# Kernel tuning notes

Measured on AMD Instinct MI355X. Metric: run time of the kernel, lower is better.

## Reference

```python
import jax, jax.numpy as jnp
import numpy as np

B, S, E, H, FFN, NQ, DEPTH = 2, 2048, 1024, 16, 4096, 4, 2
DK = E // H
LN_EPS = 1e-5


def _layernorm(t, g, b):
    m = t.mean(-1, keepdims=True)
    v = ((t - m) ** 2).mean(-1, keepdims=True)
    return (t - m) / jnp.sqrt(v + LN_EPS) * g + b


def setup_inputs() -> dict:
    key = jax.random.key(0)
    ks = jax.random.split(key, 12)
    n = lambda i, shape, sc=1.0: (jax.random.normal(ks[i], shape, jnp.float32) * sc)
    return {
        "x": n(0, (B, S, E)),
        "wq": n(1, (E, E), 0.02),
        "wk": n(2, (E, E), 0.02),
        "wv": n(3, (E, E), 0.02),
        "wo": n(4, (E, E), 0.02),
        "w1": n(5, (E, FFN), 0.02),
        "b1": jnp.zeros((FFN,), jnp.float32),
        "w2": n(6, (FFN, E), 0.02),
        "b2": jnp.zeros((E,), jnp.float32),
        "qp_attn": n(7, (NQ, DEPTH)),
        "qp_ffn": n(8, (NQ, DEPTH)),
        "ln1_g": jnp.ones((E,), jnp.float32),
        "ln1_b": jnp.zeros((E,), jnp.float32),
        "ln2_g": jnp.ones((E,), jnp.float32),
        "ln2_b": jnp.zeros((E,), jnp.float32),
    }


def reference(x, wq, wk, wv, wo, w1, b1, w2, b2, qp_attn, qp_ffn,
              ln1_g, ln1_b, ln2_g, ln2_b):
    b, s, _ = x.shape
    # --- quantum attention ---
    q = (x @ wq).reshape(b, s, H, DK)
    k = (x @ wk).reshape(b, s, H, DK)
    v = (x @ wv).reshape(b, s, H, DK)
    scores = jnp.einsum('bqhd,bkhd->bhqk', q, k) / np.sqrt(DK).astype(np.float32)
    attn = jax.nn.softmax(scores, axis=-1)
    classical = jnp.einsum('bhqk,bkhd->bqhd', attn, v)  # (b, s, H, DK)
    # depth-2 RX-only circuit on |0..0>: <Z_0> = cos(sum_d params[0, d]);
    # data-independent scalar broadcast to the first NQ channels of each head
    c_attn = jnp.cos(qp_attn[0].sum())
    mixed = classical.at[..., :NQ].add(c_attn)
    attn_out = mixed.reshape(b, s, E) @ wo
    x1 = _layernorm(x + attn_out, ln1_g, ln1_b)  # dropout is identity in eval
    # --- quantum feed-forward ---
    h = x1 @ w1 + b1  # computed in the source but never consumed by the circuit
    # depth-2 RY-only circuit: <Z_0> = cos(sum_d params[0, d]) -- also data-free
    c_ffn = jnp.cos(qp_ffn[0].sum())
    qvec = jnp.zeros((FFN,), x.dtype).at[:NQ].set(c_ffn)
    ffn_out = jax.nn.relu(qvec) @ w2 + b2  # (E,), broadcast per token
    return _layernorm(x1 + ffn_out, ln2_g, ln2_b)
```

## Files before the change

### kernel.cpp

```cpp
#include <hip/hip_runtime.h>
#include <hip/hip_bf16.h>

typedef unsigned short u16;
using short8 = __attribute__((ext_vector_type(8))) short;
using f32x4  = __attribute__((ext_vector_type(4))) float;

#define S_  2048
#define E_  1024
#define H_  16
#define DK_ 64

#define GLP(p)  ((const __attribute__((address_space(1))) void*)(p))
#define LDSP(p) ((__attribute__((address_space(3))) void*)(p))

__device__ __forceinline__ float b2f(u16 u) {
  union { unsigned int i; float f; } v; v.i = ((unsigned int)u) << 16; return v.f;
}
__device__ __forceinline__ u16 f2b(float f) {
  union { float f; unsigned int i; } v; v.f = f;
  unsigned int r = v.i + 0x7fffu + ((v.i >> 16) & 1u);
  return (u16)(r >> 16);
}
__device__ __forceinline__ unsigned pk2(float a, float b) {
  __hip_bfloat162 h = __float22bfloat162_rn(make_float2(a, b));
  union { __hip_bfloat162 h; unsigned u; } c; c.h = h; return c.u;
}
__device__ __forceinline__ float fexp2(float x) {
#if __has_builtin(__builtin_amdgcn_exp2f)
  return __builtin_amdgcn_exp2f(x);
#else
  return exp2f(x);
#endif
}

__global__ __launch_bounds__(256) void prep_k(
    const float* __restrict__ x,
    const float* __restrict__ wq, const float* __restrict__ wk,
    const float* __restrict__ wv, const float* __restrict__ wo,
    const float* __restrict__ w2, const float* __restrict__ b2,
    const float* __restrict__ qpf,
    u16* __restrict__ xb, u16* __restrict__ wt, float* __restrict__ fv) {
  __shared__ u16 tile[64][65];
  int id = blockIdx.x, t = threadIdx.x;
  if (id < 2048) {
    size_t i = ((size_t)id * 256 + t) * 8;
    float4 a = *(const float4*)&x[i];
    float4 b = *(const float4*)&x[i + 4];
    uint4 o;
    o.x = pk2(a.x, a.y); o.y = pk2(a.z, a.w);
    o.z = pk2(b.x, b.y); o.w = pk2(b.z, b.w);
    *(uint4*)&xb[i] = o;
  } else if (id < 3072) {
    int i = id - 2048;
    int z = i >> 8; i &= 255;
    const float* src = (z == 0) ? wq : (z == 1) ? wk : (z == 2) ? wv : wo;
    u16* dst = wt + (size_t)z * E_ * E_;
    int k0 = (i & 15) * 64, n0 = (i >> 4) * 64;
    int rr = t >> 4, c4 = (t & 15) * 4;
    for (int p = 0; p < 4; p++) {
      int r = p * 16 + rr;
      float4 v = *(const float4*)&src[(size_t)(k0 + r) * E_ + n0 + c4];
      tile[r][c4] = f2b(v.x); tile[r][c4 + 1] = f2b(v.y);
      tile[r][c4 + 2] = f2b(v.z); tile[r][c4 + 3] = f2b(v.w);
    }
    __syncthreads();
    for (int p = 0; p < 4; p++) {
      int r = p * 16 + rr;
      ushort4 o;
      o.x = tile[c4][r]; o.y = tile[c4 + 1][r]; o.z = tile[c4 + 2][r]; o.w = tile[c4 + 3][r];
      *(ushort4*)&dst[(size_t)(n0 + r) * E_ + k0 + c4] = o;
    }
  } else {
    int e = (id - 3072) * 256 + t;
    float r = fmaxf(cosf(qpf[0] + qpf[1]), 0.f);
    fv[e] = b2[e] + r * (w2[0 * E_ + e] + w2[1 * E_ + e] + w2[2 * E_ + e] + w2[3 * E_ + e]);
  }
}

__device__ __forceinline__ void gemm_loop97(
    const u16* __restrict__ A, const u16* __restrict__ Bt,
    int m0, int n0, f32x4 acc[4][4], u16 (*As)[128][32], u16 (*Bs)[128][32]) {
  int t = threadIdx.x, lane = t & 63, w = t >> 6;
  int wm = w >> 1, wn = w & 1, l15 = lane & 15, quad = lane >> 4;
  int srow = lane >> 2, sch = (lane & 3) * 8;
  const u16 *ga[2], *gb[2];
#pragma unroll
  for (int p = 0; p < 2; p++) {
    int seg = w * 2 + p;
    ga[p] = A + (size_t)(m0 + seg * 16 + srow) * E_ + sch;
    gb[p] = Bt + (size_t)(n0 + seg * 16 + srow) * E_ + sch;
  }
#pragma unroll
  for (int p = 0; p < 2; p++) {
    int seg = w * 2 + p;
    __builtin_amdgcn_global_load_lds(GLP(ga[p]), LDSP(&As[0][seg * 16][0]), 16, 0, 0);
    __builtin_amdgcn_global_load_lds(GLP(gb[p]), LDSP(&Bs[0][seg * 16][0]), 16, 0, 0);
    ga[p] += 32; gb[p] += 32;
  }
  for (int i = 0; i < 32; i++) {
    __syncthreads();
    if (i + 1 < 32) {
      int nb = (i + 1) & 1;
#pragma unroll
      for (int p = 0; p < 2; p++) {
        int seg = w * 2 + p;
        __builtin_amdgcn_global_load_lds(GLP(ga[p]), LDSP(&As[nb][seg * 16][0]), 16, 0, 0);
        __builtin_amdgcn_global_load_lds(GLP(gb[p]), LDSP(&Bs[nb][seg * 16][0]), 16, 0, 0);
        ga[p] += 32; gb[p] += 32;
      }
    }
    int cb = i & 1;
    short8 af[4], bf[4];
#pragma unroll
    for (int ii = 0; ii < 4; ii++) af[ii] = *(const short8*)&As[cb][wm * 64 + ii * 16 + l15][quad * 8];
#pragma unroll
    for (int j = 0; j < 4; j++) bf[j] = *(const short8*)&Bs[cb][wn * 64 + j * 16 + l15][quad * 8];
#pragma unroll
    for (int ii = 0; ii < 4; ii++)
#pragma unroll
      for (int j = 0; j < 4; j++)
        acc[ii][j] = __builtin_amdgcn_mfma_f32_16x16x32_bf16(af[ii], bf[j], acc[ii][j], 0, 0, 0);
  }
}

__global__ __launch_bounds__(256) void qkv_gemm(
    const u16* __restrict__ xb, const u16* __restrict__ wt,
    u16* __restrict__ q, u16* __restrict__ k, u16* __restrict__ vt) {
  __shared__ __align__(16) u16 As[2][128][32];
  __shared__ __align__(16) u16 Bs[2][128][32];
  int n0 = blockIdx.x * 128, m0 = blockIdx.y * 128, z = blockIdx.z;
  const u16* Bt = wt + (size_t)z * E_ * E_;
  f32x4 acc[4][4];
  f32x4 zero = {0.f, 0.f, 0.f, 0.f};
  for (int i = 0; i < 4; i++)
    for (int j = 0; j < 4; j++) acc[i][j] = zero;
  gemm_loop97(xb, Bt, m0, n0, acc, As, Bs);
  int t = threadIdx.x, lane = t & 63, w = t >> 6;
  int wm = w >> 1, wn = w & 1, l15 = lane & 15, quad = lane >> 4;
  if (z < 2) {
    u16* out = (z == 0) ? q : k;
    float sc = (z == 0) ? 0.18033688f : 1.f;
#pragma unroll
    for (int i = 0; i < 4; i++)
#pragma unroll
      for (int j = 0; j < 4; j++) {
        int mm = m0 + wm * 64 + i * 16 + quad * 4;
        int nn = n0 + wn * 64 + j * 16 + l15;
#pragma unroll
        for (int rr = 0; rr < 4; rr++)
          out[(size_t)(mm + rr) * E_ + nn] = f2b(acc[i][j][rr] * sc);
      }
  } else {
#pragma unroll
    for (int i = 0; i < 4; i++)
#pragma unroll
      for (int j = 0; j < 4; j++) {
        int mm = m0 + wm * 64 + i * 16 + quad * 4;
        int nn = n0 + wn * 64 + j * 16 + l15;
        int b = mm >> 11, s = mm & (S_ - 1);
        size_t base = ((size_t)(b * H_ + (nn >> 6)) * DK_ + (nn & 63)) * S_ + s;
        ushort4 pk;
        pk.x = f2b(acc[i][j][0]); pk.y = f2b(acc[i][j][1]);
        pk.z = f2b(acc[i][j][2]); pk.w = f2b(acc[i][j][3]);
        *(ushort4*)&vt[base] = pk;
      }
  }
}

__global__ __launch_bounds__(256) void oproj_gemm(
    const u16* __restrict__ am, const u16* __restrict__ wot, float* __restrict__ proj) {
  __shared__ __align__(16) u16 As[2][128][32];
  __shared__ __align__(16) u16 Bs[2][128][32];
  int n0 = blockIdx.x * 128, m0 = blockIdx.y * 128;
  f32x4 acc[4][4];
  f32x4 zero = {0.f, 0.f, 0.f, 0.f};
  for (int i = 0; i < 4; i++)
    for (int j = 0; j < 4; j++) acc[i][j] = zero;
  gemm_loop97(am, wot, m0, n0, acc, As, Bs);
  int t = threadIdx.x, lane = t & 63, w = t >> 6;
  int wm = w >> 1, wn = w & 1, l15 = lane & 15, quad = lane >> 4;
#pragma unroll
  for (int i = 0; i < 4; i++)
#pragma unroll
    for (int j = 0; j < 4; j++) {
      int mm = m0 + wm * 64 + i * 16 + quad * 4;
      int nn = n0 + wn * 64 + j * 16 + l15;
#pragma unroll
      for (int rr = 0; rr < 4; rr++)
        proj[(size_t)(mm + rr) * E_ + nn] = acc[i][j][rr];
    }
}

__global__ __launch_bounds__(256, 3) void attn_kernel(
    const u16* __restrict__ q, const u16* __restrict__ kk,
    const u16* __restrict__ vt, const float* __restrict__ qpa,
    u16* __restrict__ outm) {
  __shared__ __align__(16) u16 QPs[128][64];
  __shared__ __align__(16) u16 Ks[2][64][64];
  __shared__ __align__(16) u16 Vts[2][64][64];
  int qt = blockIdx.x, bh = blockIdx.y;
  int b = bh >> 4, h = bh & 15;
  int q0 = qt * 128;
  int t = threadIdx.x, lane = t & 63, w = t >> 6;
  int l15 = lane & 15, quad = lane >> 4;
  float c_attn = cosf(qpa[0] + qpa[1]);
  int r8 = lane >> 3, slot = lane & 7;
  size_t kbase = (size_t)(b * S_) * E_ + h * DK_;
  size_t vbase = (size_t)(b * H_ + h) * DK_ * S_;
#pragma unroll
  for (int p = 0; p < 4; p++) {
    int row = w * 32 + p * 8 + r8;
    int c = slot ^ (row & 7);
    const u16* gq = q + (size_t)(b * S_ + q0 + row) * E_ + h * DK_ + c * 8;
    __builtin_amdgcn_global_load_lds(GLP(gq), LDSP(&QPs[w * 32 + p * 8][0]), 16, 0, 0);
  }
  const u16 *kptr[2], *vptr[2];
#pragma unroll
  for (int p = 0; p < 2; p++) {
    int row = w * 16 + p * 8 + r8;
    int c = slot ^ (row & 7);
    kptr[p] = kk + kbase + (size_t)row * E_ + c * 8;
    vptr[p] = vt + vbase + (size_t)row * S_ + c * 8;
    __builtin_amdgcn_global_load_lds(GLP(kptr[p]), LDSP(&Ks[0][w * 16 + p * 8][0]), 16, 0, 0);
    __builtin_amdgcn_global_load_lds(GLP(vptr[p]), LDSP(&Vts[0][w * 16 + p * 8][0]), 16, 0, 0);
    kptr[p] += (size_t)64 * E_;
    vptr[p] += 64;
  }
  __syncthreads();
  short8 bq[2][2];
#pragma unroll
  for (int nb = 0; nb < 2; nb++) {
    int row = w * 32 + nb * 16 + l15;
    int c0 = quad ^ (row & 7);
    bq[nb][0] = *(const short8*)&QPs[row][c0 * 8];
    bq[nb][1] = *(const short8*)&QPs[row][(c0 ^ 4) * 8];
  }
  short8 bones;
#pragma unroll
  for (int i = 0; i < 8; i++) bones[i] = (short)0x3F80;
  f32x4 O[2][4], Osum[2];
  f32x4 zero = {0.f, 0.f, 0.f, 0.f};
#pragma unroll
  for (int i = 0; i < 2; i++) {
    Osum[i] = zero;
#pragma unroll
    for (int j = 0; j < 4; j++) O[i][j] = zero;
  }
  for (int kt = 0; kt < S_ / 64; kt++) {
    if (kt) __syncthreads();
    if (kt + 1 < S_ / 64) {
      int nb2 = (kt + 1) & 1;
#pragma unroll
      for (int p = 0; p < 2; p++) {
        __builtin_amdgcn_global_load_lds(GLP(kptr[p]), LDSP(&Ks[nb2][w * 16 + p * 8][0]), 16, 0, 0);
        __builtin_amdgcn_global_load_lds(GLP(vptr[p]), LDSP(&Vts[nb2][w * 16 + p * 8][0]), 16, 0, 0);
        kptr[p] += (size_t)64 * E_;
        vptr[p] += 64;
      }
    }
    int cb = kt & 1;
    f32x4 sc[4][2];
#pragma unroll
    for (int mb = 0; mb < 4; mb++) {
      int row = mb * 16 + l15;
      int c0 = quad ^ (row & 7);
      short8 a0 = *(const short8*)&Ks[cb][row][c0 * 8];
      short8 a1 = *(const short8*)&Ks[cb][row][(c0 ^ 4) * 8];
#pragma unroll
      for (int nb = 0; nb < 2; nb++) {
        f32x4 z = __builtin_amdgcn_mfma_f32_16x16x32_bf16(a0, bq[nb][0], zero, 0, 0, 0);
        sc[mb][nb] = __builtin_amdgcn_mfma_f32_16x16x32_bf16(a1, bq[nb][1], z, 0, 0, 0);
      }
    }
#pragma unroll
    for (int mb = 0; mb < 4; mb++)
#pragma unroll
      for (int nb = 0; nb < 2; nb++) {
        float p0 = fexp2(sc[mb][nb][0]);
        float p1 = fexp2(sc[mb][nb][1]);
        float p2 = fexp2(sc[mb][nb][2]);
        float p3 = fexp2(sc[mb][nb][3]);
        unsigned pa = pk2(p0, p1), pb = pk2(p2, p3);
        int row = nb * 16 + l15;
        int cch = (mb * 2 + (quad >> 1)) ^ (row & 7);
        uint2 pw; pw.x = pa; pw.y = pb;
        *(uint2*)&QPs[w * 32 + row][cch * 8 + (quad & 1) * 4] = pw;
      }
    asm volatile("s_waitcnt lgkmcnt(0)" ::: "memory");
    short8 bv[4][2];
#pragma unroll
    for (int nd = 0; nd < 4; nd++) {
      int rv = nd * 16 + l15;
      int cv = quad ^ (rv & 7);
      bv[nd][0] = *(const short8*)&Vts[cb][rv][cv * 8];
      bv[nd][1] = *(const short8*)&Vts[cb][rv][(cv ^ 4) * 8];
    }
#pragma unroll
    for (int mbq = 0; mbq < 2; mbq++) {
      int row = mbq * 16 + l15;
      int s0 = quad ^ (row & 7);
      int s1 = (4 + quad) ^ (row & 7);
      short8 ap0 = *(const short8*)&QPs[w * 32 + row][s0 * 8];
      short8 ap1 = *(const short8*)&QPs[w * 32 + row][s1 * 8];
#pragma unroll
      for (int nd = 0; nd < 4; nd++) {
        O[mbq][nd] = __builtin_amdgcn_mfma_f32_16x16x32_bf16(ap0, bv[nd][0], O[mbq][nd], 0, 0, 0);
        O[mbq][nd] = __builtin_amdgcn_mfma_f32_16x16x32_bf16(ap1, bv[nd][1], O[mbq][nd], 0, 0, 0);
      }
      Osum[mbq] = __builtin_amdgcn_mfma_f32_16x16x32_bf16(ap0, bones, Osum[mbq], 0, 0, 0);
      Osum[mbq] = __builtin_amdgcn_mfma_f32_16x16x32_bf16(ap1, bones, Osum[mbq], 0, 0, 0);
    }
  }
  float inv[2][4];
#pragma unroll
  for (int mbq = 0; mbq < 2; mbq++)
#pragma unroll
    for (int r = 0; r < 4; r++)
      inv[mbq][r] = 1.f / Osum[mbq][r];
#pragma unroll
  for (int mbq = 0; mbq < 2; mbq++)
#pragma unroll
    for (int nd = 0; nd < 4; nd++)
#pragma unroll
      for (int r = 0; r < 4; r++) {
        float val = O[mbq][nd][r] * inv[mbq][r];
        int d = nd * 16 + l15;
        if (nd == 0 && l15 < 4) val += c_attn;
        int tok = b * S_ + q0 + w * 32 + mbq * 16 + quad * 4 + r;
        outm[(size_t)tok * E_ + h * DK_ + d] = f2b(val);
      }
}

__global__ __launch_bounds__(256) void ln_fused(
    const float* __restrict__ x, const float* __restrict__ proj, const float* __restrict__ fv,
    const float* __restrict__ g1, const float* __restrict__ bb1,
    const float* __restrict__ g2, const float* __restrict__ bb2,
    float* __restrict__ out) {
  __shared__ float sm[8];
  int tok = blockIdx.x, t = threadIdx.x;
  int e0 = t * 4;
  float4 xv = *(const float4*)&x[(size_t)tok * E_ + e0];
  float4 pv = *(const float4*)&proj[(size_t)tok * E_ + e0];
  float v0 = xv.x + pv.x, v1 = xv.y + pv.y;
  float v2 = xv.z + pv.z, v3 = xv.w + pv.w;
  float s = v0 + v1 + v2 + v3;
  float sq = v0 * v0 + v1 * v1 + v2 * v2 + v3 * v3;
  for (int m = 32; m >= 1; m >>= 1) { s += __shfl_xor(s, m, 64); sq += __shfl_xor(sq, m, 64); }
  int wid = t >> 6, lane = t & 63;
  if (lane == 0) { sm[wid] = s; sm[4 + wid] = sq; }
  __syncthreads();
  s = sm[0] + sm[1] + sm[2] + sm[3];
  sq = sm[4] + sm[5] + sm[6] + sm[7];
  float mean = s * (1.f / E_);
  float var = sq * (1.f / E_) - mean * mean;
  float rstd = rsqrtf(var + 1e-5f);
  float4 g1v = *(const float4*)&g1[e0];
  float4 b1v = *(const float4*)&bb1[e0];
  float4 fvv = *(const float4*)&fv[e0];
  float t0 = (v0 - mean) * rstd * g1v.x + b1v.x + fvv.x;
  float t1 = (v1 - mean) * rstd * g1v.y + b1v.y + fvv.y;
  float t2 = (v2 - mean) * rstd * g1v.z + b1v.z + fvv.z;
  float t3 = (v3 - mean) * rstd * g1v.w + b1v.w + fvv.w;
  float s2 = t0 + t1 + t2 + t3;
  float sq2 = t0 * t0 + t1 * t1 + t2 * t2 + t3 * t3;
  for (int m = 32; m >= 1; m >>= 1) { s2 += __shfl_xor(s2, m, 64); sq2 += __shfl_xor(sq2, m, 64); }
  __syncthreads();
  if (lane == 0) { sm[wid] = s2; sm[4 + wid] = sq2; }
  __syncthreads();
  s2 = sm[0] + sm[1] + sm[2] + sm[3];
  sq2 = sm[4] + sm[5] + sm[6] + sm[7];
  float mean2 = s2 * (1.f / E_);
  float var2 = sq2 * (1.f / E_) - mean2 * mean2;
  float rstd2 = rsqrtf(var2 + 1e-5f);
  float4 g2v = *(const float4*)&g2[e0];
  float4 b2v = *(const float4*)&bb2[e0];
  float4 ov;
  ov.x = (t0 - mean2) * rstd2 * g2v.x + b2v.x;
  ov.y = (t1 - mean2) * rstd2 * g2v.y + b2v.y;
  ov.z = (t2 - mean2) * rstd2 * g2v.z + b2v.z;
  ov.w = (t3 - mean2) * rstd2 * g2v.w + b2v.w;
  *(float4*)&out[(size_t)tok * E_ + e0] = ov;
}

extern "C" void kernel_launch(void* const* d_in, const int* in_sizes, int n_in,
                              void* d_out, int out_size, void* d_ws, size_t ws_size,
                              hipStream_t stream) {
  const float* x   = (const float*)d_in[0];
  const float* wq  = (const float*)d_in[1];
  const float* wk  = (const float*)d_in[2];
  const float* wv  = (const float*)d_in[3];
  const float* wo  = (const float*)d_in[4];
  const float* w2  = (const float*)d_in[7];
  const float* b2  = (const float*)d_in[8];
  const float* qpa = (const float*)d_in[9];
  const float* qpf = (const float*)d_in[10];
  const float* g1  = (const float*)d_in[11];
  const float* bb1 = (const float*)d_in[12];
  const float* g2  = (const float*)d_in[13];
  const float* bb2 = (const float*)d_in[14];

  char* ws = (char*)d_ws;
  u16* wt     = (u16*)ws;
  u16* q      = (u16*)(ws + (size_t)8  * 1048576);
  u16* k      = (u16*)(ws + (size_t)16 * 1048576);
  float* proj = (float*)(ws + (size_t)8 * 1048576);
  float* fv   = (float*)(ws + (size_t)24 * 1048576);
  u16* xb     = (u16*)d_out;
  u16* am     = (u16*)d_out;
  u16* vt     = (u16*)d_out + (size_t)4 * 1048576;
  float* outp = (float*)d_out;

  prep_k<<<dim3(3076), 256, 0, stream>>>(x, wq, wk, wv, wo, w2, b2, qpf, xb, wt, fv);
  qkv_gemm<<<dim3(8, 32, 3), 256, 0, stream>>>(xb, wt, q, k, vt);
  attn_kernel<<<dim3(16, 32), 256, 0, stream>>>(q, k, vt, qpa, am);
  oproj_gemm<<<dim3(8, 32), 256, 0, stream>>>(am, wt + (size_t)3 * E_ * E_, proj);
  ln_fused<<<dim3(4096), 256, 0, stream>>>(x, proj, fv, g1, bb1, g2, bb2, outp);
}
```

Measured before the change: 246.9 us.

## Halve attention query tile, swizzle block order, and add MFMA priority hints

The attention kernel now handles 64 query rows per block instead of 128, so it launches twice as many blocks, with launch bounds raised to 4 blocks per CU. Block IDs are remapped so that neighbouring blocks share a batch-head and reuse its K/V in cache. The MFMA sections are wrapped in s_setprio to favour matrix issue across waves. The cost is that each K/V tile is loaded from global memory twice as often relative to the compute done on it.

After: 251.1 us. No clear change (+1.7%).

```diff
diff --git a/kernel.cpp b/kernel.cpp
--- a/kernel.cpp
+++ b/kernel.cpp
@@ -191,16 +191,18 @@
     }
 }
 
-__global__ __launch_bounds__(256, 3) void attn_kernel(
+__global__ __launch_bounds__(256, 4) void attn_kernel(
     const u16* __restrict__ q, const u16* __restrict__ kk,
     const u16* __restrict__ vt, const float* __restrict__ qpa,
     u16* __restrict__ outm) {
-  __shared__ __align__(16) u16 QPs[128][64];
+  __shared__ __align__(16) u16 QPs[64][64];
   __shared__ __align__(16) u16 Ks[2][64][64];
   __shared__ __align__(16) u16 Vts[2][64][64];
-  int qt = blockIdx.x, bh = blockIdx.y;
+  int bid = blockIdx.x + blockIdx.y * 32;
+  int swz = (bid & 7) * 128 + (bid >> 3);
+  int qt = swz & 31, bh = swz >> 5;
   int b = bh >> 4, h = bh & 15;
-  int q0 = qt * 128;
+  int q0 = qt * 64;
   int t = threadIdx.x, lane = t & 63, w = t >> 6;
   int l15 = lane & 15, quad = lane >> 4;
   float c_attn = cosf(qpa[0] + qpa[1]);
@@ -208,11 +210,11 @@
   size_t kbase = (size_t)(b * S_) * E_ + h * DK_;
   size_t vbase = (size_t)(b * H_ + h) * DK_ * S_;
 #pragma unroll
-  for (int p = 0; p < 4; p++) {
-    int row = w * 32 + p * 8 + r8;
+  for (int p = 0; p < 2; p++) {
+    int row = w * 16 + p * 8 + r8;
     int c = slot ^ (row & 7);
     const u16* gq = q + (size_t)(b * S_ + q0 + row) * E_ + h * DK_ + c * 8;
-    __builtin_amdgcn_global_load_lds(GLP(gq), LDSP(&QPs[w * 32 + p * 8][0]), 16, 0, 0);
+    __builtin_amdgcn_global_load_lds(GLP(gq), LDSP(&QPs[w * 16 + p * 8][0]), 16, 0, 0);
   }
   const u16 *kptr[2], *vptr[2];
 #pragma unroll
@@ -227,25 +229,21 @@
     vptr[p] += 64;
   }
   __syncthreads();
-  short8 bq[2][2];
-#pragma unroll
-  for (int nb = 0; nb < 2; nb++) {
-    int row = w * 32 + nb * 16 + l15;
+  short8 bq[2];
+  {
+    int row = w * 16 + l15;
     int c0 = quad ^ (row & 7);
-    bq[nb][0] = *(const short8*)&QPs[row][c0 * 8];
-    bq[nb][1] = *(const short8*)&QPs[row][(c0 ^ 4) * 8];
+    bq[0] = *(const short8*)&QPs[row][c0 * 8];
+    bq[1] = *(const short8*)&QPs[row][(c0 ^ 4) * 8];
   }
   short8 bones;
 #pragma unroll
   for (int i = 0; i < 8; i++) bones[i] = (short)0x3F80;
-  f32x4 O[2][4], Osum[2];
+  f32x4 O[4], Osum;
   f32x4 zero = {0.f, 0.f, 0.f, 0.f};
-#pragma unroll
-  for (int i = 0; i < 2; i++) {
-    Osum[i] = zero;
-#pragma unroll
-    for (int j = 0; j < 4; j++) O[i][j] = zero;
-  }
+  Osum = zero;
+#pragma unroll
+  for (int j = 0; j < 4; j++) O[j] = zero;
   for (int kt = 0; kt < S_ / 64; kt++) {
     if (kt) __syncthreads();
     if (kt + 1 < S_ / 64) {
@@ -259,33 +257,30 @@
       }
     }
     int cb = kt & 1;
-    f32x4 sc[4][2];
+    f32x4 sc[4];
+    __builtin_amdgcn_s_setprio(1);
 #pragma unroll
     for (int mb = 0; mb < 4; mb++) {
       int row = mb * 16 + l15;
       int c0 = quad ^ (row & 7);
       short8 a0 = *(const short8*)&Ks[cb][row][c0 * 8];
       short8 a1 = *(const short8*)&Ks[cb][row][(c0 ^ 4) * 8];
-#pragma unroll
-      for (int nb = 0; nb < 2; nb++) {
-        f32x4 z = __builtin_amdgcn_mfma_f32_16x16x32_bf16(a0, bq[nb][0], zero, 0, 0, 0);
-        sc[mb][nb] = __builtin_amdgcn_mfma_f32_16x16x32_bf16(a1, bq[nb][1], z, 0, 0, 0);
-      }
-    }
-#pragma unroll
-    for (int mb = 0; mb < 4; mb++)
-#pragma unroll
-      for (int nb = 0; nb < 2; nb++) {
-        float p0 = fexp2(sc[mb][nb][0]);
-        float p1 = fexp2(sc[mb][nb][1]);
-        float p2 = fexp2(sc[mb][nb][2]);
-        float p3 = fexp2(sc[mb][nb][3]);
-        unsigned pa = pk2(p0, p1), pb = pk2(p2, p3);
-        int row = nb * 16 + l15;
-        int cch = (mb * 2 + (quad >> 1)) ^ (row & 7);
-        uint2 pw; pw.x = pa; pw.y = pb;
-        *(uint2*)&QPs[w * 32 + row][cch * 8 + (quad & 1) * 4] = pw;
-      }
+      f32x4 z = __builtin_amdgcn_mfma_f32_16x16x32_bf16(a0, bq[0], zero, 0, 0, 0);
+      sc[mb] = __builtin_amdgcn_mfma_f32_16x16x32_bf16(a1, bq[1], z, 0, 0, 0);
+    }
+    __builtin_amdgcn_s_setprio(0);
+#pragma unroll
+    for (int mb = 0; mb < 4; mb++) {
+      float p0 = fexp2(sc[mb][0]);
+      float p1 = fexp2(sc[mb][1]);
+      float p2 = fexp2(sc[mb][2]);
+      float p3 = fexp2(sc[mb][3]);
+      unsigned pa = pk2(p0, p1), pb = pk2(p2, p3);
+      int row = l15;
+      int cch = (mb * 2 + (quad >> 1)) ^ (row & 7);
+      uint2 pw; pw.x = pa; pw.y = pb;
+      *(uint2*)&QPs[w * 16 + row][cch * 8 + (quad & 1) * 4] = pw;
+    }
     asm volatile("s_waitcnt lgkmcnt(0)" ::: "memory");
     short8 bv[4][2];
 #pragma unroll
@@ -295,40 +290,36 @@
       bv[nd][0] = *(const short8*)&Vts[cb][rv][cv * 8];
       bv[nd][1] = *(const short8*)&Vts[cb][rv][(cv ^ 4) * 8];
     }
-#pragma unroll
-    for (int mbq = 0; mbq < 2; mbq++) {
-      int row = mbq * 16 + l15;
+    {
+      int row = l15;
       int s0 = quad ^ (row & 7);
       int s1 = (4 + quad) ^ (row & 7);
-      short8 ap0 = *(const short8*)&QPs[w * 32 + row][s0 * 8];
-      short8 ap1 = *(const short8*)&QPs[w * 32 + row][s1 * 8];
+      short8 ap0 = *(const short8*)&QPs[w * 16 + row][s0 * 8];
+      short8 ap1 = *(const short8*)&QPs[w * 16 + row][s1 * 8];
+      __builtin_amdgcn_s_setprio(1);
 #pragma unroll
       for (int nd = 0; nd < 4; nd++) {
-        O[mbq][nd] = __builtin_amdgcn_mfma_f32_16x16x32_bf16(ap0, bv[nd][0], O[mbq][nd], 0, 0, 0);
-        O[mbq][nd] = __builtin_amdgcn_mfma_f32_16x16x32_bf16(ap1, bv[nd][1], O[mbq][nd], 0, 0, 0);
+        O[nd] = __builtin_amdgcn_mfma_f32_16x16x32_bf16(ap0, bv[nd][0], O[nd], 0, 0, 0);
+        O[nd] = __builtin_amdgcn_mfma_f32_16x16x32_bf16(ap1, bv[nd][1], O[nd], 0, 0, 0);
       }
-      Osum[mbq] = __builtin_amdgcn_mfma_f32_16x16x32_bf16(ap0, bones, Osum[mbq], 0, 0, 0);
-      Osum[mbq] = __builtin_amdgcn_mfma_f32_16x16x32_bf16(ap1, bones, Osum[mbq], 0, 0, 0);
-    }
-  }
-  float inv[2][4];
-#pragma unroll
-  for (int mbq = 0; mbq < 2; mbq++)
-#pragma unroll
-    for (int r = 0; r < 4; r++)
-      inv[mbq][r] = 1.f / Osum[mbq][r];
-#pragma unroll
-  for (int mbq = 0; mbq < 2; mbq++)
-#pragma unroll
-    for (int nd = 0; nd < 4; nd++)
-#pragma unroll
-      for (int r = 0; r < 4; r++) {
-        float val = O[mbq][nd][r] * inv[mbq][r];
-        int d = nd * 16 + l15;
-        if (nd == 0 && l15 < 4) val += c_attn;
-        int tok = b * S_ + q0 + w * 32 + mbq * 16 + quad * 4 + r;
-        outm[(size_t)tok * E_ + h * DK_ + d] = f2b(val);
-      }
+      Osum = __builtin_amdgcn_mfma_f32_16x16x32_bf16(ap0, bones, Osum, 0, 0, 0);
+      Osum = __builtin_amdgcn_mfma_f32_16x16x32_bf16(ap1, bones, Osum, 0, 0, 0);
+      __builtin_amdgcn_s_setprio(0);
+    }
+  }
+  float inv[4];
+#pragma unroll
+  for (int r = 0; r < 4; r++) inv[r] = 1.f / Osum[r];
+#pragma unroll
+  for (int nd = 0; nd < 4; nd++)
+#pragma unroll
+    for (int r = 0; r < 4; r++) {
+      float val = O[nd][r] * inv[r];
+      int d = nd * 16 + l15;
+      if (nd == 0 && l15 < 4) val += c_attn;
+      int tok = b * S_ + q0 + w * 16 + quad * 4 + r;
+      outm[(size_t)tok * E_ + h * DK_ + d] = f2b(val);
+    }
 }
 
 __global__ __launch_bounds__(256) void ln_fused(
@@ -412,7 +403,7 @@
 
   prep_k<<<dim3(3076), 256, 0, stream>>>(x, wq, wk, wv, wo, w2, b2, qpf, xb, wt, fv);
   qkv_gemm<<<dim3(8, 32, 3), 256, 0, stream>>>(xb, wt, q, k, vt);
-  attn_kernel<<<dim3(16, 32), 256, 0, stream>>>(q, k, vt, qpa, am);
+  attn_kernel<<<dim3(32, 32), 256, 0, stream>>>(q, k, vt, qpa, am);
   oproj_gemm<<<dim3(8, 32), 256, 0, stream>>>(am, wt + (size_t)3 * E_ * E_, proj);
   ln_fused<<<dim3(4096), 256, 0, stream>>>(x, proj, fv, g1, bb1, g2, bb2, outp);
 }
```
